# Kernel optimization log

Measured on AMD Instinct MI355X. Metric: run time of the kernel, lower is better.

The kernel has to match this reference:

```python
import jax, jax.numpy as jnp
import numpy as np

HEADS = 16
HEAD_DIM = 64  # embed_size // heads = 1024 // 16


def setup_inputs() -> dict:
    key = jax.random.key(0)
    ks = jax.random.split(key, 9)
    N, Sq, E, C = 4, 2048, 1024, 512
    Skv = 2 * Sq  # keys/values seq must equal doubled query seq (see view trick)
    return {
        "values": jax.random.normal(ks[0], (N, Skv, E), dtype=jnp.float32),
        "keys": jax.random.normal(ks[1], (N, Skv, E), dtype=jnp.float32),
        "queries": jax.random.normal(ks[2], (N, Sq, E), dtype=jnp.float32),
        "mask": jax.random.randint(ks[3], (N, Skv, HEADS, HEADS), 0, 2, dtype=jnp.int32),
        "condition": jax.random.normal(ks[4], (N, Sq, C), dtype=jnp.float32),
        "Wc": jax.random.normal(ks[5], (E, C), dtype=jnp.float32) * 0.02,
        "bc": jax.random.normal(ks[6], (E,), dtype=jnp.float32) * 0.02,
        "Wo": jax.random.normal(ks[7], (E, E), dtype=jnp.float32) * 0.02,
        "bo": jax.random.normal(ks[8], (E,), dtype=jnp.float32) * 0.02,
    }


def reference(values, keys, queries, mask, condition, Wc, bc, Wo, bo):
    N = queries.shape[0]
    H, D = HEADS, HEAD_DIM
    # condition_linear + concat: (N, Sq, 2E) -> view doubles seq -> (N, 2Sq, H, D)
    cond_feat = jnp.einsum('nsc,ec->nse', condition, Wc) + bc
    cq = jnp.concatenate([queries, cond_feat], axis=-1).reshape(N, -1, H, D)
    k = keys.reshape(N, -1, H, D)    # (N, 2Sq, H, D)
    v = values.reshape(N, -1, H, D)  # (N, 2Sq, H, D)
    # per-(batch,seq) heads-by-heads attention, exactly as the torch matmul does
    att = jnp.einsum('nshd,nsed->nshe', cq, k) / jnp.sqrt(jnp.float32(D))
    att = jnp.where(mask == 0, jnp.float32(-1e20), att)
    att = jax.nn.softmax(att, axis=-1)
    out = jnp.einsum('nshe,nsed->nshd', att, v).reshape(N, -1, H * D)
    return jnp.einsum('nsk,ek->nse', out, Wo) + bo
```

## Files before the change

kernel.cpp:

```cpp
#include <hip/hip_runtime.h>
#include <hip/hip_bf16.h>
#include <type_traits>

#define NB   4
#define SQ   2048
#define SKV  4096
#define EMB  1024
#define CDIM 512

typedef __attribute__((ext_vector_type(8))) short short8;
typedef __attribute__((ext_vector_type(4))) float f32x4;

__device__ __forceinline__ float b2f(ushort u) {
    union { unsigned int i; float f; } v;
    v.i = ((unsigned int)u) << 16;
    return v.f;
}
__device__ __forceinline__ ushort f2b(float f) {
    union { float f; unsigned int i; } v; v.f = f;
    unsigned int x = v.i;
    return (ushort)((x + 0x7fffu + ((x >> 16) & 1u)) >> 16);
}

__device__ __forceinline__ void glds16(const ushort* gp, ushort* lp) {
    __builtin_amdgcn_global_load_lds(
        (const __attribute__((address_space(1))) unsigned int*)gp,
        (__attribute__((address_space(3))) unsigned int*)lp,
        16, 0, 0);
}

__global__ __launch_bounds__(256)
void cvt_f32_bf16(const float* __restrict__ in, ushort* __restrict__ out, int n4)
{
    const int i = blockIdx.x * 256 + threadIdx.x;
    if (i < n4) {
        float4 v = ((const float4*)in)[i];
        ushort4 o;
        o.x = f2b(v.x); o.y = f2b(v.y); o.z = f2b(v.z); o.w = f2b(v.w);
        ((ushort4*)out)[i] = o;
    }
}

template <typename OT>
__global__ __launch_bounds__(256)
void gemm_bt_bias(const ushort* __restrict__ A, const ushort* __restrict__ B,
                  const float* __restrict__ bias, OT* __restrict__ C,
                  int M, int Nn, int K)
{
    __shared__ __attribute__((aligned(16))) ushort As[128 * 32];
    __shared__ __attribute__((aligned(16))) ushort Bs[128 * 32];

    const int tid  = threadIdx.x;
    const int wave = tid >> 6;
    const int lane = tid & 63;
    const int quad = lane >> 4;
    const int l16  = lane & 15;
    const int wr   = wave >> 1;
    const int wc   = wave & 1;

    const long mBase = (long)blockIdx.x * 128;
    const long nBase = (long)blockIdx.y * 128;

    const ushort* Ablk = A + mBase * K;
    const ushort* Bblk = B + nBase * K;

    const int lr = lane >> 2;
    const int lc = (lane & 3) * 8;
    const int c0 = wave * 2, c1 = wave * 2 + 1;
    const ushort* aG0 = Ablk + (long)(c0 * 16 + lr) * K + lc;
    const ushort* aG1 = Ablk + (long)(c1 * 16 + lr) * K + lc;
    const ushort* bG0 = Bblk + (long)(c0 * 16 + lr) * K + lc;
    const ushort* bG1 = Bblk + (long)(c1 * 16 + lr) * K + lc;
    ushort* aL0 = As + c0 * 512;
    ushort* aL1 = As + c1 * 512;
    ushort* bL0 = Bs + c0 * 512;
    ushort* bL1 = Bs + c1 * 512;

    f32x4 acc[4][4];
#pragma unroll
    for (int i = 0; i < 4; ++i)
#pragma unroll
        for (int j = 0; j < 4; ++j)
            acc[i][j] = (f32x4){0.f, 0.f, 0.f, 0.f};

    for (int k0 = 0; k0 < K; k0 += 32) {
        __syncthreads();
        glds16(aG0 + k0, aL0);
        glds16(aG1 + k0, aL1);
        glds16(bG0 + k0, bL0);
        glds16(bG1 + k0, bL1);
        __syncthreads();

        short8 af[4], bfr[4];
#pragma unroll
        for (int mt = 0; mt < 4; ++mt)
            af[mt] = *(const short8*)(As + (wr * 64 + mt * 16 + l16) * 32 + quad * 8);
#pragma unroll
        for (int nt = 0; nt < 4; ++nt)
            bfr[nt] = *(const short8*)(Bs + (wc * 64 + nt * 16 + l16) * 32 + quad * 8);

#pragma unroll
        for (int mt = 0; mt < 4; ++mt)
#pragma unroll
            for (int nt = 0; nt < 4; ++nt)
                acc[mt][nt] = __builtin_amdgcn_mfma_f32_16x16x32_bf16(
                    af[mt], bfr[nt], acc[mt][nt], 0, 0, 0);
    }

#pragma unroll
    for (int mt = 0; mt < 4; ++mt) {
#pragma unroll
        for (int nt = 0; nt < 4; ++nt) {
            const long n = nBase + wc * 64 + nt * 16 + l16;
            const float bv = bias[n];
#pragma unroll
            for (int r = 0; r < 4; ++r) {
                const long m = mBase + wr * 64 + mt * 16 + quad * 4 + r;
                if constexpr (std::is_same<OT, float>::value)
                    C[m * Nn + n] = acc[mt][nt][r] + bv;
                else
                    C[m * Nn + n] = f2b(acc[mt][nt][r] + bv);
            }
        }
    }
}

__global__ __launch_bounds__(256)
void attn_kernel(const float*  __restrict__ queries,
                 const ushort* __restrict__ condfeat,
                 const float*  __restrict__ keys,
                 const float*  __restrict__ values,
                 const int*    __restrict__ mask,
                 ushort* __restrict__ attout)
{
    const int pos = blockIdx.x;
    const int s2  = pos & 4095;
    const int n   = pos >> 12;
    const int tid = threadIdx.x;

    __shared__ __attribute__((aligned(16))) float cq[16 * 68];
    __shared__ __attribute__((aligned(16))) float ks[16 * 68];
    __shared__ __attribute__((aligned(16))) float vs[16 * 68];
    __shared__ float sc[16 * 17];

    {
        const int base = tid * 4;
        const int h = base >> 6, d = base & 63;
        float4 q4;
        if (s2 & 1) {
            const ushort* cp = condfeat + ((size_t)n * SQ + (s2 >> 1)) * EMB + base;
            ushort4 c4 = *(const ushort4*)cp;
            q4.x = b2f(c4.x); q4.y = b2f(c4.y); q4.z = b2f(c4.z); q4.w = b2f(c4.w);
        } else {
            q4 = *(const float4*)(queries + ((size_t)n * SQ + (s2 >> 1)) * EMB + base);
        }
        float4 k4 = *(const float4*)(keys   + (size_t)pos * EMB + base);
        float4 v4 = *(const float4*)(values + (size_t)pos * EMB + base);
        *(float4*)(cq + h * 68 + d) = q4;
        *(float4*)(ks + h * 68 + d) = k4;
        *(float4*)(vs + h * 68 + d) = v4;
    }
    __syncthreads();

    {
        const int h = tid >> 4, e = tid & 15;
        float s = 0.f;
#pragma unroll
        for (int d = 0; d < 64; d += 4) {
            float4 a = *(const float4*)(cq + h * 68 + d);
            float4 b = *(const float4*)(ks + e * 68 + d);
            s += a.x * b.x + a.y * b.y + a.z * b.z + a.w * b.w;
        }
        s *= 0.125f;
        const int mv = mask[(size_t)pos * 256 + tid];
        s = (mv == 0) ? -1e20f : s;

        float mx = s;
#pragma unroll
        for (int d = 1; d < 16; d <<= 1)
            mx = fmaxf(mx, __shfl_xor(mx, d));
        const float ex = __expf(s - mx);
        float sum = ex;
#pragma unroll
        for (int d = 1; d < 16; d <<= 1)
            sum += __shfl_xor(sum, d);
        sc[h * 17 + e] = ex / sum;
    }
    __syncthreads();

    {
        const int idx = tid * 4;
        const int h = idx >> 6, d0 = idx & 63;
        float4 a = {0.f, 0.f, 0.f, 0.f};
#pragma unroll
        for (int e = 0; e < 16; ++e) {
            const float p = sc[h * 17 + e];
            float4 v4 = *(const float4*)(vs + e * 68 + d0);
            a.x += p * v4.x; a.y += p * v4.y; a.z += p * v4.z; a.w += p * v4.w;
        }
        ushort4 o;
        o.x = f2b(a.x); o.y = f2b(a.y); o.z = f2b(a.z); o.w = f2b(a.w);
        *(ushort4*)(attout + (size_t)pos * EMB + idx) = o;
    }
}

extern "C" void kernel_launch(void* const* d_in, const int* in_sizes, int n_in,
                              void* d_out, int out_size, void* d_ws, size_t ws_size,
                              hipStream_t stream)
{
    const float* values    = (const float*)d_in[0];
    const float* keys      = (const float*)d_in[1];
    const float* queries   = (const float*)d_in[2];
    const int*   mask      = (const int*)  d_in[3];
    const float* condition = (const float*)d_in[4];
    const float* Wc        = (const float*)d_in[5];
    const float* bc        = (const float*)d_in[6];
    const float* Wo        = (const float*)d_in[7];
    const float* bo        = (const float*)d_in[8];
    float* out = (float*)d_out;

    ushort* condfeat = (ushort*)d_ws;
    ushort* attout   = condfeat + (size_t)NB * SQ * EMB;
    ushort* cond_bf  = attout;
    ushort* Wc_bf    = attout + (size_t)NB * SQ * CDIM;
    ushort* Wo_bf    = condfeat;

    cvt_f32_bf16<<<(NB * SQ * CDIM / 4 + 255) / 256, 256, 0, stream>>>(
        condition, cond_bf, NB * SQ * CDIM / 4);
    cvt_f32_bf16<<<(EMB * CDIM / 4 + 255) / 256, 256, 0, stream>>>(
        Wc, Wc_bf, EMB * CDIM / 4);

    {
        dim3 grid((NB * SQ) / 128, EMB / 128);
        gemm_bt_bias<ushort><<<grid, 256, 0, stream>>>(
            cond_bf, Wc_bf, bc, condfeat, NB * SQ, EMB, CDIM);
    }

    attn_kernel<<<NB * SKV, 256, 0, stream>>>(queries, condfeat, keys, values,
                                              mask, attout);

    cvt_f32_bf16<<<(EMB * EMB / 4 + 255) / 256, 256, 0, stream>>>(
        Wo, Wo_bf, EMB * EMB / 4);

    {
        dim3 grid((NB * SKV) / 128, EMB / 128);
        gemm_bt_bias<float><<<grid, 256, 0, stream>>>(
            attout, Wo_bf, bo, out, NB * SKV, EMB, EMB);
    }
}
```

Before: 303.0 us.

## Process several positions per attention block with double-buffered async LDS loads

Each attention block now handles 8 sequence positions instead of one. Q/K/V rows for the next position are loaded directly into LDS with global_load_lds into a second buffer while the current position is computed. LDS uses an XOR-swizzled layout in place of padding, and the softmax probabilities travel to the PV step by wave shuffles instead of an LDS round trip and extra barrier. The goal is to hide global-load latency and cut per-block launch and sync overhead, at the price of 8x fewer blocks (2048), which may reduce memory-level parallelism.

```diff
diff --git a/kernel.cpp b/kernel.cpp
--- a/kernel.cpp
+++ b/kernel.cpp
@@ -7,6 +7,7 @@
 #define SKV  4096
 #define EMB  1024
 #define CDIM 512
+#define PPB  8
 
 typedef __attribute__((ext_vector_type(8))) short short8;
 typedef __attribute__((ext_vector_type(4))) float f32x4;
@@ -133,46 +134,63 @@
                  const int*    __restrict__ mask,
                  ushort* __restrict__ attout)
 {
-    const int pos = blockIdx.x;
-    const int s2  = pos & 4095;
-    const int n   = pos >> 12;
-    const int tid = threadIdx.x;
-
-    __shared__ __attribute__((aligned(16))) float cq[16 * 68];
-    __shared__ __attribute__((aligned(16))) float ks[16 * 68];
-    __shared__ __attribute__((aligned(16))) float vs[16 * 68];
-    __shared__ float sc[16 * 17];
-
-    {
-        const int base = tid * 4;
-        const int h = base >> 6, d = base & 63;
-        float4 q4;
-        if (s2 & 1) {
-            const ushort* cp = condfeat + ((size_t)n * SQ + (s2 >> 1)) * EMB + base;
-            ushort4 c4 = *(const ushort4*)cp;
-            q4.x = b2f(c4.x); q4.y = b2f(c4.y); q4.z = b2f(c4.z); q4.w = b2f(c4.w);
+    __shared__ __attribute__((aligned(16))) float cqb[2][1024];
+    __shared__ __attribute__((aligned(16))) float kb [2][1024];
+    __shared__ __attribute__((aligned(16))) float vb [2][1024];
+
+    const int tid  = threadIdx.x;
+    const int wave = tid >> 6;
+    const int lane = tid & 63;
+    const int h    = tid >> 4;
+    const int e    = tid & 15;
+    const int basePos = blockIdx.x * PPB;
+
+    const int r   = tid >> 4;
+    const int c4s = ((tid & 15) ^ (r & 7)) << 2;
+
+    auto stage = [&](int p, int b) {
+        const size_t rowOff = ((size_t)p << 10) + (size_t)((r << 6) + c4s);
+        glds16((const ushort*)(keys   + rowOff), (ushort*)&kb[b][wave << 8]);
+        glds16((const ushort*)(values + rowOff), (ushort*)&vb[b][wave << 8]);
+        const int n  = p >> 12;
+        const int sh = (p & 4095) >> 1;
+        if (p & 1) {
+            if (tid < 128) {
+                const int rr = tid >> 3, c8 = tid & 7;
+                glds16(condfeat + (((size_t)n * SQ + sh) << 10)
+                                + (size_t)((rr << 6) + ((c8 ^ (rr & 7)) << 3)),
+                       (ushort*)&cqb[b][0] + (wave << 9));
+            }
         } else {
-            q4 = *(const float4*)(queries + ((size_t)n * SQ + (s2 >> 1)) * EMB + base);
-        }
-        float4 k4 = *(const float4*)(keys   + (size_t)pos * EMB + base);
-        float4 v4 = *(const float4*)(values + (size_t)pos * EMB + base);
-        *(float4*)(cq + h * 68 + d) = q4;
-        *(float4*)(ks + h * 68 + d) = k4;
-        *(float4*)(vs + h * 68 + d) = v4;
-    }
-    __syncthreads();
-
-    {
-        const int h = tid >> 4, e = tid & 15;
+            glds16((const ushort*)(queries + (((size_t)n * SQ + sh) << 10)
+                                           + (size_t)((r << 6) + c4s)),
+                   (ushort*)&cqb[b][wave << 8]);
+        }
+    };
+
+    auto compute = [&](int p, int b, int mv) {
         float s = 0.f;
-#pragma unroll
-        for (int d = 0; d < 64; d += 4) {
-            float4 a = *(const float4*)(cq + h * 68 + d);
-            float4 b = *(const float4*)(ks + e * 68 + d);
-            s += a.x * b.x + a.y * b.y + a.z * b.z + a.w * b.w;
+        if (p & 1) {
+            const ushort* cq = (const ushort*)&cqb[b][0];
+#pragma unroll
+            for (int d8 = 0; d8 < 8; ++d8) {
+                short8 qv = *(const short8*)(cq + (h << 6) + ((d8 ^ (h & 7)) << 3));
+                float4 k0 = *(const float4*)&kb[b][(e << 6) + (((2 * d8)     ^ (e & 7)) << 2)];
+                float4 k1 = *(const float4*)&kb[b][(e << 6) + (((2 * d8 + 1) ^ (e & 7)) << 2)];
+                s += b2f((ushort)qv[0]) * k0.x + b2f((ushort)qv[1]) * k0.y
+                   + b2f((ushort)qv[2]) * k0.z + b2f((ushort)qv[3]) * k0.w
+                   + b2f((ushort)qv[4]) * k1.x + b2f((ushort)qv[5]) * k1.y
+                   + b2f((ushort)qv[6]) * k1.z + b2f((ushort)qv[7]) * k1.w;
+            }
+        } else {
+#pragma unroll
+            for (int d4 = 0; d4 < 16; ++d4) {
+                float4 qv = *(const float4*)&cqb[b][(h << 6) + ((d4 ^ (h & 7)) << 2)];
+                float4 kv = *(const float4*)&kb [b][(e << 6) + ((d4 ^ (e & 7)) << 2)];
+                s += qv.x * kv.x + qv.y * kv.y + qv.z * kv.z + qv.w * kv.w;
+            }
         }
         s *= 0.125f;
-        const int mv = mask[(size_t)pos * 256 + tid];
         s = (mv == 0) ? -1e20f : s;
 
         float mx = s;
@@ -184,23 +202,35 @@
 #pragma unroll
         for (int d = 1; d < 16; d <<= 1)
             sum += __shfl_xor(sum, d);
-        sc[h * 17 + e] = ex / sum;
-    }
+        const float pr = ex / sum;
+
+        f32x4 acc = (f32x4){0.f, 0.f, 0.f, 0.f};
+        const int sb = lane & 48;
+#pragma unroll
+        for (int ee = 0; ee < 16; ++ee) {
+            const float pe = __shfl(pr, sb | ee);
+            float4 v4 = *(const float4*)&vb[b][(ee << 6) + (((tid & 15) ^ (ee & 7)) << 2)];
+            acc[0] += pe * v4.x; acc[1] += pe * v4.y;
+            acc[2] += pe * v4.z; acc[3] += pe * v4.w;
+        }
+        ushort4 o;
+        o.x = f2b(acc[0]); o.y = f2b(acc[1]); o.z = f2b(acc[2]); o.w = f2b(acc[3]);
+        *(ushort4*)(attout + ((size_t)p << 10) + (tid << 2)) = o;
+    };
+
+    stage(basePos, 0);
+    int mvN = mask[((size_t)basePos << 8) + tid];
     __syncthreads();
 
-    {
-        const int idx = tid * 4;
-        const int h = idx >> 6, d0 = idx & 63;
-        float4 a = {0.f, 0.f, 0.f, 0.f};
-#pragma unroll
-        for (int e = 0; e < 16; ++e) {
-            const float p = sc[h * 17 + e];
-            float4 v4 = *(const float4*)(vs + e * 68 + d0);
-            a.x += p * v4.x; a.y += p * v4.y; a.z += p * v4.z; a.w += p * v4.w;
-        }
-        ushort4 o;
-        o.x = f2b(a.x); o.y = f2b(a.y); o.z = f2b(a.z); o.w = f2b(a.w);
-        *(ushort4*)(attout + (size_t)pos * EMB + idx) = o;
+#pragma unroll
+    for (int i = 0; i < PPB; ++i) {
+        const int mv = mvN;
+        if (i + 1 < PPB) {
+            stage(basePos + i + 1, (i + 1) & 1);
+            mvN = mask[((size_t)(basePos + i + 1) << 8) + tid];
+        }
+        compute(basePos + i, i & 1, mv);
+        __syncthreads();
     }
 }
 
@@ -236,8 +266,8 @@
             cond_bf, Wc_bf, bc, condfeat, NB * SQ, EMB, CDIM);
     }
 
-    attn_kernel<<<NB * SKV, 256, 0, stream>>>(queries, condfeat, keys, values,
-                                              mask, attout);
+    attn_kernel<<<(NB * SKV) / PPB, 256, 0, stream>>>(queries, condfeat, keys,
+                                                      values, mask, attout);
 
     cvt_f32_bf16<<<(EMB * EMB / 4 + 255) / 256, 256, 0, stream>>>(
         Wo, Wo_bf, EMB * EMB / 4);
```

After: 314.4 us. 3.7% more time.

## Process several positions per attention block with register prefetch; remap GEMM tile order

Applied to the files above, without the earlier changes.

The attention kernel now handles four sequence positions per block, loading the next position's q/k/v/mask into registers while computing the current one, so global load latency overlaps with compute and per-block launch overhead is amortised. The GEMM kernel also remaps block indices so consecutive blocks are grouped by chiplet-sized chunks of M tiles across all N tiles, aiming for better L2 reuse of A rows. The trade-offs are a quarter as many attention blocks, an extra barrier per position, and more registers held for the prefetch.

```diff
diff --git a/kernel.cpp b/kernel.cpp
--- a/kernel.cpp
+++ b/kernel.cpp
@@ -7,6 +7,7 @@
 #define SKV  4096
 #define EMB  1024
 #define CDIM 512
+#define POS  4
 
 typedef __attribute__((ext_vector_type(8))) short short8;
 typedef __attribute__((ext_vector_type(4))) float f32x4;
@@ -58,8 +59,20 @@
     const int wr   = wave >> 1;
     const int wc   = wave & 1;
 
-    const long mBase = (long)blockIdx.x * 128;
-    const long nBase = (long)blockIdx.y * 128;
+    int mTile, nTile;
+    {
+        const int gx = gridDim.x, gy = gridDim.y;
+        const int flat = blockIdx.y * gx + blockIdx.x;
+        if ((gx & 7) == 0 && gy == 8) {
+            const int c = flat & 7, j = flat >> 3;
+            mTile = c * (gx >> 3) + (j >> 3);
+            nTile = j & 7;
+        } else {
+            mTile = blockIdx.x; nTile = blockIdx.y;
+        }
+    }
+    const long mBase = (long)mTile * 128;
+    const long nBase = (long)nTile * 128;
 
     const ushort* Ablk = A + mBase * K;
     const ushort* Bblk = B + nBase * K;
@@ -133,74 +146,95 @@
                  const int*    __restrict__ mask,
                  ushort* __restrict__ attout)
 {
-    const int pos = blockIdx.x;
-    const int s2  = pos & 4095;
-    const int n   = pos >> 12;
-    const int tid = threadIdx.x;
+    const int tid     = threadIdx.x;
+    const int basePos = blockIdx.x * POS;
 
     __shared__ __attribute__((aligned(16))) float cq[16 * 68];
     __shared__ __attribute__((aligned(16))) float ks[16 * 68];
     __shared__ __attribute__((aligned(16))) float vs[16 * 68];
     __shared__ float sc[16 * 17];
 
-    {
-        const int base = tid * 4;
-        const int h = base >> 6, d = base & 63;
+    const int base4 = tid * 4;
+    const int hs = base4 >> 6, dsd = base4 & 63;
+
+    auto loadQ = [&](int p) -> float4 {
+        const int n = p >> 12, sh = (p & 4095) >> 1;
         float4 q4;
-        if (s2 & 1) {
-            const ushort* cp = condfeat + ((size_t)n * SQ + (s2 >> 1)) * EMB + base;
+        if (p & 1) {
+            const ushort* cp = condfeat + ((size_t)n * SQ + sh) * EMB + base4;
             ushort4 c4 = *(const ushort4*)cp;
             q4.x = b2f(c4.x); q4.y = b2f(c4.y); q4.z = b2f(c4.z); q4.w = b2f(c4.w);
         } else {
-            q4 = *(const float4*)(queries + ((size_t)n * SQ + (s2 >> 1)) * EMB + base);
-        }
-        float4 k4 = *(const float4*)(keys   + (size_t)pos * EMB + base);
-        float4 v4 = *(const float4*)(values + (size_t)pos * EMB + base);
-        *(float4*)(cq + h * 68 + d) = q4;
-        *(float4*)(ks + h * 68 + d) = k4;
-        *(float4*)(vs + h * 68 + d) = v4;
-    }
-    __syncthreads();
-
-    {
-        const int h = tid >> 4, e = tid & 15;
-        float s = 0.f;
-#pragma unroll
-        for (int d = 0; d < 64; d += 4) {
-            float4 a = *(const float4*)(cq + h * 68 + d);
-            float4 b = *(const float4*)(ks + e * 68 + d);
-            s += a.x * b.x + a.y * b.y + a.z * b.z + a.w * b.w;
-        }
-        s *= 0.125f;
-        const int mv = mask[(size_t)pos * 256 + tid];
-        s = (mv == 0) ? -1e20f : s;
-
-        float mx = s;
-#pragma unroll
-        for (int d = 1; d < 16; d <<= 1)
-            mx = fmaxf(mx, __shfl_xor(mx, d));
-        const float ex = __expf(s - mx);
-        float sum = ex;
-#pragma unroll
-        for (int d = 1; d < 16; d <<= 1)
-            sum += __shfl_xor(sum, d);
-        sc[h * 17 + e] = ex / sum;
-    }
-    __syncthreads();
-
-    {
-        const int idx = tid * 4;
-        const int h = idx >> 6, d0 = idx & 63;
-        float4 a = {0.f, 0.f, 0.f, 0.f};
-#pragma unroll
-        for (int e = 0; e < 16; ++e) {
-            const float p = sc[h * 17 + e];
-            float4 v4 = *(const float4*)(vs + e * 68 + d0);
-            a.x += p * v4.x; a.y += p * v4.y; a.z += p * v4.z; a.w += p * v4.w;
-        }
-        ushort4 o;
-        o.x = f2b(a.x); o.y = f2b(a.y); o.z = f2b(a.z); o.w = f2b(a.w);
-        *(ushort4*)(attout + (size_t)pos * EMB + idx) = o;
+            q4 = *(const float4*)(queries + ((size_t)n * SQ + sh) * EMB + base4);
+        }
+        return q4;
+    };
+
+    float4 q4 = loadQ(basePos);
+    float4 k4 = *(const float4*)(keys   + ((size_t)basePos << 10) + base4);
+    float4 v4 = *(const float4*)(values + ((size_t)basePos << 10) + base4);
+    int    mv = mask[((size_t)basePos << 8) + tid];
+
+#pragma unroll
+    for (int i = 0; i < POS; ++i) {
+        const int p = basePos + i;
+
+        *(float4*)(cq + hs * 68 + dsd) = q4;
+        *(float4*)(ks + hs * 68 + dsd) = k4;
+        *(float4*)(vs + hs * 68 + dsd) = v4;
+        __syncthreads();
+
+        float4 q4n, k4n, v4n; int mvn = 0;
+        if (i + 1 < POS) {
+            q4n = loadQ(p + 1);
+            k4n = *(const float4*)(keys   + ((size_t)(p + 1) << 10) + base4);
+            v4n = *(const float4*)(values + ((size_t)(p + 1) << 10) + base4);
+            mvn = mask[((size_t)(p + 1) << 8) + tid];
+        }
+
+        {
+            const int h = tid >> 4, e = tid & 15;
+            float s = 0.f;
+#pragma unroll
+            for (int d = 0; d < 64; d += 4) {
+                float4 a = *(const float4*)(cq + h * 68 + d);
+                float4 b = *(const float4*)(ks + e * 68 + d);
+                s += a.x * b.x + a.y * b.y + a.z * b.z + a.w * b.w;
+            }
+            s *= 0.125f;
+            s = (mv == 0) ? -1e20f : s;
+
+            float mx = s;
+#pragma unroll
+            for (int d = 1; d < 16; d <<= 1)
+                mx = fmaxf(mx, __shfl_xor(mx, d));
+            const float ex = __expf(s - mx);
+            float sum = ex;
+#pragma unroll
+            for (int d = 1; d < 16; d <<= 1)
+                sum += __shfl_xor(sum, d);
+            sc[h * 17 + e] = ex / sum;
+        }
+        __syncthreads();
+
+        {
+            float4 a = {0.f, 0.f, 0.f, 0.f};
+#pragma unroll
+            for (int e = 0; e < 16; ++e) {
+                const float pe = sc[hs * 17 + e];
+                float4 vv = *(const float4*)(vs + e * 68 + dsd);
+                a.x += pe * vv.x; a.y += pe * vv.y;
+                a.z += pe * vv.z; a.w += pe * vv.w;
+            }
+            ushort4 o;
+            o.x = f2b(a.x); o.y = f2b(a.y); o.z = f2b(a.z); o.w = f2b(a.w);
+            *(ushort4*)(attout + ((size_t)p << 10) + base4) = o;
+        }
+
+        if (i + 1 < POS) {
+            __syncthreads();
+            q4 = q4n; k4 = k4n; v4 = v4n; mv = mvn;
+        }
     }
 }
 
@@ -236,8 +270,8 @@
             cond_bf, Wc_bf, bc, condfeat, NB * SQ, EMB, CDIM);
     }
 
-    attn_kernel<<<NB * SKV, 256, 0, stream>>>(queries, condfeat, keys, values,
-                                              mask, attout);
+    attn_kernel<<<(NB * SKV) / POS, 256, 0, stream>>>(queries, condfeat, keys,
+                                                      values, mask, attout);
 
     cvt_f32_bf16<<<(EMB * EMB / 4 + 255) / 256, 256, 0, stream>>>(
         Wo, Wo_bf, EMB * EMB / 4);
```

New measurement: 311.8 us. +2.9%, slower.
